# Kernel optimization log

Hardware: AMD Instinct MI355X
Metric: run time of the kernel (lower is better)

The kernel has to match this reference:

```python
import jax, jax.numpy as jnp
import numpy as np
import math

D_MODEL = 1024
NUM_HEAD = 16
HEAD_DIM = D_MODEL // NUM_HEAD
B, S = 4, 2048


def setup_inputs() -> dict:
    key = jax.random.key(0)
    k1, k2, k3, k4, k5 = jax.random.split(key, 5)
    x = jax.random.normal(k1, (B, S, D_MODEL), dtype=jnp.float32)
    # causal mask: True = position masked out
    mask = jnp.triu(jnp.ones((S, S), dtype=bool), k=1)[None, None, :, :]
    sc = 1.0 / math.sqrt(D_MODEL)
    w_q = jax.random.normal(k2, (D_MODEL, D_MODEL), dtype=jnp.float32) * sc
    w_k = jax.random.normal(k3, (D_MODEL, D_MODEL), dtype=jnp.float32) * sc
    w_v = jax.random.normal(k4, (D_MODEL, D_MODEL), dtype=jnp.float32) * sc
    w_out = jax.random.normal(k5, (D_MODEL, D_MODEL), dtype=jnp.float32) * sc
    return {"x": x, "mask": mask, "w_q": w_q, "w_k": w_k, "w_v": w_v, "w_out": w_out}


def reference(x, mask, w_q, w_k, w_v, w_out):
    b, s, _ = x.shape
    # nn.Linear applies x @ W.T; weights stored as [out, in]
    q = jnp.einsum('bsd,ed->bse', x, w_q).reshape(b, s, NUM_HEAD, HEAD_DIM).transpose(0, 2, 1, 3)
    k = jnp.einsum('bsd,ed->bse', x, w_k).reshape(b, s, NUM_HEAD, HEAD_DIM).transpose(0, 2, 1, 3)
    v = jnp.einsum('bsd,ed->bse', x, w_v).reshape(b, s, NUM_HEAD, HEAD_DIM).transpose(0, 2, 1, 3)
    # NOTE: faithful to source - scales by 1/sqrt(d_model), not 1/sqrt(head_dim)
    q = q / jnp.sqrt(jnp.asarray(D_MODEL, dtype=q.dtype))
    attn_weight = jnp.einsum('bhqd,bhkd->bhqk', q, k)  # [B,H,S,S]
    attn_weight = jnp.where(mask, jnp.asarray(-1e9, dtype=attn_weight.dtype), attn_weight)
    attn_weight = jax.nn.softmax(attn_weight, axis=-1)
    attn = jnp.einsum('bhqk,bhkd->bhqd', attn_weight, v)
    attn = attn.transpose(0, 2, 1, 3).reshape(b, s, D_MODEL)
    out = jnp.einsum('bsd,ed->bse', attn, w_out)
    return out
```

## Files before the change

### kernel.cpp

```cpp
#include <hip/hip_runtime.h>

#define BDIM 4
#define SDIM 2048
#define DMODEL 1024
#define NHEAD 16
#define HDIM 64
#define MTOT (BDIM*SDIM)

typedef unsigned short u16;
typedef unsigned int u32;
typedef __attribute__((ext_vector_type(8))) short bf16x8;
typedef __attribute__((ext_vector_type(4))) float f32x4;
typedef __attribute__((ext_vector_type(16))) float f32x16;
typedef __attribute__((ext_vector_type(4))) u32 u32x4;

__device__ __forceinline__ u16 f2bf(float f) {
  unsigned u = __builtin_bit_cast(unsigned, f);
  u += 0x7fffu + ((u >> 16) & 1u);
  return (u16)(u >> 16);
}

__device__ __forceinline__ u32 cvtpk(float a, float b) {
  u32 r;
  asm("v_cvt_pk_bf16_f32 %0, %1, %2" : "=v"(r) : "v"(a), "v"(b));
  return r;
}

__device__ __forceinline__ void gload_lds16(const u16* g, u16* l) {
  __builtin_amdgcn_global_load_lds(
      (const __attribute__((address_space(1))) unsigned int*)g,
      (__attribute__((address_space(3))) unsigned int*)l, 16, 0, 0);
}

__global__ __launch_bounds__(256) void cast_bf16_kernel(
    const float* __restrict__ src, u16* __restrict__ dst, int n4)
{
  const int i = blockIdx.x * 256 + threadIdx.x;
  if (i < n4) {
    const float4 v = reinterpret_cast<const float4*>(src)[i];
    unsigned long long w =
        (unsigned long long)f2bf(v.x)
      | ((unsigned long long)f2bf(v.y) << 16)
      | ((unsigned long long)f2bf(v.z) << 32)
      | ((unsigned long long)f2bf(v.w) << 48);
    reinterpret_cast<unsigned long long*>(dst)[i] = w;
  }
}

__global__ __launch_bounds__(256) void gemm_bf16_kernel(
    const u16* __restrict__ A, const u16* __restrict__ W,
    void* __restrict__ C, float scale, int mode)
{
  __shared__ u16 As[2][128 * 32];
  __shared__ u16 Bs[2][128 * 32];

  const int tid = threadIdx.x;
  const int m0 = blockIdx.y * 128, n0 = blockIdx.x * 128;
  const int l  = tid & 63, wid = tid >> 6;
  const int wr = wid >> 1, wc = wid & 1;
  const int lc = l & 15, lr = l >> 4;
  const int ar = l >> 2;
  const int ac = (l & 3) * 8;

  const f32x4 z4 = {0.f, 0.f, 0.f, 0.f};
  f32x4 acc[4][4];
  #pragma unroll
  for (int i = 0; i < 4; ++i)
    #pragma unroll
    for (int j = 0; j < 4; ++j) acc[i][j] = z4;

  #define GSTAGE(bufi, kk)                                                        \
    { _Pragma("unroll")                                                           \
      for (int j = 0; j < 2; ++j) {                                               \
        const int row = wid * 32 + j * 16;                                        \
        gload_lds16(&A[(size_t)(m0 + row + ar) * DMODEL + (kk) + ac],             \
                    &As[bufi][row * 32]);                                         \
        gload_lds16(&W[(size_t)(n0 + row + ar) * DMODEL + (kk) + ac],             \
                    &Bs[bufi][row * 32]);                                         \
      } }

  GSTAGE(0, 0);
  __syncthreads();

  for (int ks = 0; ks < DMODEL / 32; ++ks) {
    const int cur = ks & 1;
    if (ks + 1 < DMODEL / 32) GSTAGE(cur ^ 1, (ks + 1) * 32);

    bf16x8 a[4], b[4];
    #pragma unroll
    for (int i = 0; i < 4; ++i)
      a[i] = *reinterpret_cast<const bf16x8*>(&As[cur][(wr*64 + i*16 + lc) * 32 + lr*8]);
    #pragma unroll
    for (int j = 0; j < 4; ++j)
      b[j] = *reinterpret_cast<const bf16x8*>(&Bs[cur][(wc*64 + j*16 + lc) * 32 + lr*8]);

    #pragma unroll
    for (int i = 0; i < 4; ++i)
      #pragma unroll
      for (int j = 0; j < 4; ++j)
        acc[i][j] = __builtin_amdgcn_mfma_f32_16x16x32_bf16(a[i], b[j], acc[i][j], 0, 0, 0);
    __syncthreads();
  }
  #undef GSTAGE

  #pragma unroll
  for (int mi = 0; mi < 4; ++mi)
    #pragma unroll
    for (int ni = 0; ni < 4; ++ni) {
      const int col = n0 + wc*64 + ni*16 + lc;
      #pragma unroll
      for (int j = 0; j < 4; ++j) {
        const int row = m0 + wr*64 + mi*16 + lr*4 + j;
        const float v = acc[mi][ni][j] * scale;
        if (mode == 0) {
          reinterpret_cast<float*>(C)[(size_t)row * DMODEL + col] = v;
        } else if (mode == 1) {
          const int b = row >> 11, s = row & (SDIM-1), h = col >> 6, dh = col & 63;
          reinterpret_cast<u16*>(C)[(((size_t)(b*NHEAD + h) * SDIM + s) << 6) + dh] = f2bf(v);
        } else {
          const int b = row >> 11, s = row & (SDIM-1), h = col >> 6, dh = col & 63;
          reinterpret_cast<u16*>(C)[(((size_t)(b*NHEAD + h) * HDIM + dh) << 11) + s] = f2bf(v);
        }
      }
    }
}

__global__ __launch_bounds__(256, 3) void attn_mfma_kernel(
    const u16* __restrict__ Qh, const u16* __restrict__ Kh,
    const u16* __restrict__ Vt, u16* __restrict__ Ob)
{
  __shared__ u16 Ks[2][64 * 64];
  __shared__ u16 Vs[2][64 * 64];

  const int tid = threadIdx.x, l = tid & 63, wid = tid >> 6;
  const int q31 = l & 31, hi = l >> 5;
  const int qt = (int)gridDim.x - 1 - (int)blockIdx.x;
  const int bh = blockIdx.y;
  const size_t base = (size_t)bh * SDIM * HDIM;
  const int qrow0 = qt * 128 + wid * 32;

  const int sr = l >> 3;
  const int sc = ((l & 7) ^ sr) * 8;

  bf16x8 aq[4];
  #pragma unroll
  for (int kc = 0; kc < 4; ++kc)
    aq[kc] = *reinterpret_cast<const bf16x8*>(
        &Qh[base + (size_t)(qrow0 + q31) * HDIM + kc*16 + hi*8]);

  f32x16 o[2], p[2];
  #pragma unroll
  for (int r = 0; r < 16; ++r) { o[0][r] = 0.f; o[1][r] = 0.f; }
  float m_run = -1e30f, l_run = 0.f;

  #define STAGE(bufi, kv0s)                                                     \
    { _Pragma("unroll")                                                         \
      for (int j = 0; j < 2; ++j) {                                             \
        const int rg = wid * 16 + j * 8;                                        \
        gload_lds16(&Kh[base + (size_t)((kv0s) + rg + sr) * HDIM + sc],         \
                    &Ks[bufi][rg * 64]);                                        \
        gload_lds16(&Vt[base + (size_t)(rg + sr) * SDIM + (kv0s) + sc],         \
                    &Vs[bufi][rg * 64]);                                        \
      } }

  const int nt = 2 * qt + 2;
  STAGE(0, 0);
  __syncthreads();

  for (int t = 0; t < nt; ++t) {
    const int kv0 = t * 64;
    const int cur = t & 1;
    if (t + 1 < nt) STAGE(cur ^ 1, kv0 + 64);

    if (kv0 <= qrow0 + 31) {
      #pragma unroll
      for (int kvb = 0; kvb < 2; ++kvb) {
        #pragma unroll
        for (int r = 0; r < 16; ++r) p[kvb][r] = 0.f;
        const int krow = kvb*32 + q31;
        #pragma unroll
        for (int kc = 0; kc < 4; ++kc) {
          const int byte = (krow*128 + kc*32 + hi*16) ^ ((krow & 7) << 4);
          const bf16x8 ak = *reinterpret_cast<const bf16x8*>(
              reinterpret_cast<const char*>(Ks[cur]) + byte);
          p[kvb] = __builtin_amdgcn_mfma_f32_32x32x16_bf16(ak, aq[kc], p[kvb], 0, 0, 0);
        }
      }

      if (kv0 + 63 > qrow0) {
        const int q = qrow0 + q31;
        #pragma unroll
        for (int kvb = 0; kvb < 2; ++kvb)
          #pragma unroll
          for (int r = 0; r < 16; ++r) {
            const int kv = kv0 + kvb*32 + (r & 3) + 8*(r >> 2) + 4*hi;
            if (kv > q) p[kvb][r] = -1e9f;
          }
      }

      float pm = -1e30f;
      #pragma unroll
      for (int r = 0; r < 16; ++r) {
        pm = fmaxf(pm, p[0][r]); pm = fmaxf(pm, p[1][r]);
      }
      pm = fmaxf(pm, __shfl_xor(pm, 32));
      float mn = m_run;
      if (!__all(pm - m_run <= 8.0f)) {
        mn = fmaxf(m_run, pm);
        const float al = __builtin_amdgcn_exp2f(m_run - mn);
        #pragma unroll
        for (int r = 0; r < 16; ++r) { o[0][r] *= al; o[1][r] *= al; }
        l_run *= al;
        m_run = mn;
      }
      float rs = 0.f;
      #pragma unroll
      for (int kvb = 0; kvb < 2; ++kvb)
        #pragma unroll
        for (int r = 0; r < 16; ++r) {
          const float e = __builtin_amdgcn_exp2f(p[kvb][r] - mn);
          p[kvb][r] = e; rs += e;
        }
      rs += __shfl_xor(rs, 32);
      l_run += rs;

      bf16x8 pb[4];
      #pragma unroll
      for (int kvb = 0; kvb < 2; ++kvb)
        #pragma unroll
        for (int s2 = 0; s2 < 2; ++s2) {
          const int rb = s2 * 8;
          const u32 k01 = cvtpk(p[kvb][rb+0], p[kvb][rb+1]);
          const u32 k23 = cvtpk(p[kvb][rb+2], p[kvb][rb+3]);
          const u32 k45 = cvtpk(p[kvb][rb+4], p[kvb][rb+5]);
          const u32 k67 = cvtpk(p[kvb][rb+6], p[kvb][rb+7]);
          const u32 sa = hi ? k01 : k45;
          const u32 sb = hi ? k23 : k67;
          const u32 ra = (u32)__shfl_xor((int)sa, 32);
          const u32 rb2 = (u32)__shfl_xor((int)sb, 32);
          u32x4 w;
          w.x = hi ? ra  : k01;
          w.y = hi ? rb2 : k23;
          w.z = hi ? k45 : ra;
          w.w = hi ? k67 : rb2;
          pb[kvb*2 + s2] = __builtin_bit_cast(bf16x8, w);
        }

      #pragma unroll
      for (int db = 0; db < 2; ++db) {
        const int vrow = db*32 + q31;
        #pragma unroll
        for (int s = 0; s < 4; ++s) {
          const int byte = (vrow*128 + s*32 + hi*16) ^ ((vrow & 7) << 4);
          const bf16x8 av = *reinterpret_cast<const bf16x8*>(
              reinterpret_cast<const char*>(Vs[cur]) + byte);
          o[db] = __builtin_amdgcn_mfma_f32_32x32x16_bf16(av, pb[s], o[db], 0, 0, 0);
        }
      }
    }
    __syncthreads();
  }
  #undef STAGE

  const float inv = 1.0f / l_run;
  char* const myOb = reinterpret_cast<char*>(reinterpret_cast<u16*>(Ks) + wid * 2048);
  #pragma unroll
  for (int db = 0; db < 2; ++db)
    #pragma unroll
    for (int tq = 0; tq < 4; ++tq) {
      const int d0 = db*32 + tq*8 + hi*4;
      uint2 wv;
      wv.x = cvtpk(o[db][tq*4+0] * inv, o[db][tq*4+1] * inv);
      wv.y = cvtpk(o[db][tq*4+2] * inv, o[db][tq*4+3] * inv);
      const int byte = (q31*128 + d0*2) ^ ((q31 & 7) << 4);
      *reinterpret_cast<uint2*>(myOb + byte) = wv;
    }
  __syncthreads();
  const int b = bh >> 4, h = bh & 15;
  const int qr = l >> 1, half = l & 1;
  const int qg = qrow0 + qr;
  #pragma unroll
  for (int i = 0; i < 4; ++i) {
    const int byte = (qr*128 + half*64 + i*16) ^ ((qr & 7) << 4);
    const u32x4 v = *reinterpret_cast<const u32x4*>(myOb + byte);
    *reinterpret_cast<u32x4*>(
        &Ob[((size_t)(b * SDIM + qg)) * DMODEL + h * HDIM + half*32 + i*8]) = v;
  }
}

extern "C" void kernel_launch(void* const* d_in, const int* in_sizes, int n_in,
                              void* d_out, int out_size, void* d_ws, size_t ws_size,
                              hipStream_t stream) {
  const float* x     = (const float*)d_in[0];
  const float* w_q   = (const float*)d_in[2];
  const float* w_k   = (const float*)d_in[3];
  const float* w_v   = (const float*)d_in[4];
  const float* w_out = (const float*)d_in[5];
  float* out = (float*)d_out;

  const size_t NX = (size_t)MTOT * DMODEL;
  const size_t NW = (size_t)DMODEL * DMODEL;
  u16* xb   = (u16*)d_ws;
  u16* wqb  = xb  + NX;
  u16* wkb  = wqb + NW;
  u16* wvb  = wkb + NW;
  u16* wob  = wvb + NW;
  u16* Qhd  = wob + NW;
  u16* Khd  = Qhd + NX;
  u16* Vtd  = Khd + NX;
  u16* attb = Vtd + NX;

  cast_bf16_kernel<<<(int)(NX/4 + 255)/256, 256, 0, stream>>>(x, xb, (int)(NX/4));
  cast_bf16_kernel<<<(int)(NW/4 + 255)/256, 256, 0, stream>>>(w_q,   wqb, (int)(NW/4));
  cast_bf16_kernel<<<(int)(NW/4 + 255)/256, 256, 0, stream>>>(w_k,   wkb, (int)(NW/4));
  cast_bf16_kernel<<<(int)(NW/4 + 255)/256, 256, 0, stream>>>(w_v,   wvb, (int)(NW/4));
  cast_bf16_kernel<<<(int)(NW/4 + 255)/256, 256, 0, stream>>>(w_out, wob, (int)(NW/4));

  const dim3 gg(DMODEL / 128, MTOT / 128);
  gemm_bf16_kernel<<<gg, 256, 0, stream>>>(xb, wqb, Qhd, 1.4426950408889634f / 32.0f, 1);
  gemm_bf16_kernel<<<gg, 256, 0, stream>>>(xb, wkb, Khd, 1.0f, 1);
  gemm_bf16_kernel<<<gg, 256, 0, stream>>>(xb, wvb, Vtd, 1.0f, 2);

  attn_mfma_kernel<<<dim3(SDIM / 128, BDIM * NHEAD), 256, 0, stream>>>(Qhd, Khd, Vtd, attb);

  gemm_bf16_kernel<<<gg, 256, 0, stream>>>(attb, wob, out, 1.0f, 0);
}
```

Measured before the change: 364.1 us.

## Batch weight casts and QKV GEMMs, swizzle tiles, add MFMA priority hints

```diff
diff --git a/kernel.cpp b/kernel.cpp
--- a/kernel.cpp
+++ b/kernel.cpp
@@ -47,15 +47,34 @@
   }
 }
 
-__global__ __launch_bounds__(256) void gemm_bf16_kernel(
+__global__ __launch_bounds__(256) void cast_w4_kernel(
+    const float* __restrict__ w0, const float* __restrict__ w1,
+    const float* __restrict__ w2, const float* __restrict__ w3,
+    u16* __restrict__ d0, u16* __restrict__ d1,
+    u16* __restrict__ d2, u16* __restrict__ d3, int n4)
+{
+  const int y = blockIdx.y;
+  const float* src = (y == 0) ? w0 : (y == 1) ? w1 : (y == 2) ? w2 : w3;
+  u16* dst = (y == 0) ? d0 : (y == 1) ? d1 : (y == 2) ? d2 : d3;
+  const int i = blockIdx.x * 256 + threadIdx.x;
+  if (i < n4) {
+    const float4 v = reinterpret_cast<const float4*>(src)[i];
+    unsigned long long w =
+        (unsigned long long)f2bf(v.x)
+      | ((unsigned long long)f2bf(v.y) << 16)
+      | ((unsigned long long)f2bf(v.z) << 32)
+      | ((unsigned long long)f2bf(v.w) << 48);
+    reinterpret_cast<unsigned long long*>(dst)[i] = w;
+  }
+}
+
+template <int MODE>
+__device__ __forceinline__ void gemm_tile(
     const u16* __restrict__ A, const u16* __restrict__ W,
-    void* __restrict__ C, float scale, int mode)
-{
-  __shared__ u16 As[2][128 * 32];
-  __shared__ u16 Bs[2][128 * 32];
-
+    void* __restrict__ C, float scale, int m0, int n0,
+    u16* As , u16* Bs )
+{
   const int tid = threadIdx.x;
-  const int m0 = blockIdx.y * 128, n0 = blockIdx.x * 128;
   const int l  = tid & 63, wid = tid >> 6;
   const int wr = wid >> 1, wc = wid & 1;
   const int lc = l & 15, lr = l >> 4;
@@ -74,9 +93,9 @@
       for (int j = 0; j < 2; ++j) {                                               \
         const int row = wid * 32 + j * 16;                                        \
         gload_lds16(&A[(size_t)(m0 + row + ar) * DMODEL + (kk) + ac],             \
-                    &As[bufi][row * 32]);                                         \
+                    &As[(bufi) * 4096 + row * 32]);                               \
         gload_lds16(&W[(size_t)(n0 + row + ar) * DMODEL + (kk) + ac],             \
-                    &Bs[bufi][row * 32]);                                         \
+                    &Bs[(bufi) * 4096 + row * 32]);                               \
       } }
 
   GSTAGE(0, 0);
@@ -89,16 +108,18 @@
     bf16x8 a[4], b[4];
     #pragma unroll
     for (int i = 0; i < 4; ++i)
-      a[i] = *reinterpret_cast<const bf16x8*>(&As[cur][(wr*64 + i*16 + lc) * 32 + lr*8]);
+      a[i] = *reinterpret_cast<const bf16x8*>(&As[cur*4096 + (wr*64 + i*16 + lc) * 32 + lr*8]);
     #pragma unroll
     for (int j = 0; j < 4; ++j)
-      b[j] = *reinterpret_cast<const bf16x8*>(&Bs[cur][(wc*64 + j*16 + lc) * 32 + lr*8]);
-
+      b[j] = *reinterpret_cast<const bf16x8*>(&Bs[cur*4096 + (wc*64 + j*16 + lc) * 32 + lr*8]);
+
+    __builtin_amdgcn_s_setprio(1);
     #pragma unroll
     for (int i = 0; i < 4; ++i)
       #pragma unroll
       for (int j = 0; j < 4; ++j)
         acc[i][j] = __builtin_amdgcn_mfma_f32_16x16x32_bf16(a[i], b[j], acc[i][j], 0, 0, 0);
+    __builtin_amdgcn_s_setprio(0);
     __syncthreads();
   }
   #undef GSTAGE
@@ -112,9 +133,9 @@
       for (int j = 0; j < 4; ++j) {
         const int row = m0 + wr*64 + mi*16 + lr*4 + j;
         const float v = acc[mi][ni][j] * scale;
-        if (mode == 0) {
+        if (MODE == 0) {
           reinterpret_cast<float*>(C)[(size_t)row * DMODEL + col] = v;
-        } else if (mode == 1) {
+        } else if (MODE == 1) {
           const int b = row >> 11, s = row & (SDIM-1), h = col >> 6, dh = col & 63;
           reinterpret_cast<u16*>(C)[(((size_t)(b*NHEAD + h) * SDIM + s) << 6) + dh] = f2bf(v);
         } else {
@@ -125,7 +146,40 @@
     }
 }
 
-__global__ __launch_bounds__(256, 3) void attn_mfma_kernel(
+__device__ __forceinline__ void swz_tile(int& m0, int& n0) {
+  const int lin = blockIdx.y * 8 + blockIdx.x;
+  const int swz = (lin & 7) * 64 + (lin >> 3);
+  m0 = (swz >> 3) * 128;
+  n0 = (swz & 7) * 128;
+}
+
+__global__ __launch_bounds__(256) void gemm_qkv_kernel(
+    const u16* __restrict__ xb,
+    const u16* __restrict__ wq, const u16* __restrict__ wk, const u16* __restrict__ wv,
+    u16* __restrict__ Qhd, u16* __restrict__ Khd, u16* __restrict__ Vtd)
+{
+  __shared__ u16 As[2 * 128 * 32];
+  __shared__ u16 Bs[2 * 128 * 32];
+  int m0, n0; swz_tile(m0, n0);
+  const int z = blockIdx.z;
+  if (z == 0)
+    gemm_tile<1>(xb, wq, Qhd, 1.4426950408889634f / 32.0f, m0, n0, As, Bs);
+  else if (z == 1)
+    gemm_tile<1>(xb, wk, Khd, 1.0f, m0, n0, As, Bs);
+  else
+    gemm_tile<2>(xb, wv, Vtd, 1.0f, m0, n0, As, Bs);
+}
+
+__global__ __launch_bounds__(256) void gemm_out_kernel(
+    const u16* __restrict__ A, const u16* __restrict__ W, float* __restrict__ C)
+{
+  __shared__ u16 As[2 * 128 * 32];
+  __shared__ u16 Bs[2 * 128 * 32];
+  int m0, n0; swz_tile(m0, n0);
+  gemm_tile<0>(A, W, C, 1.0f, m0, n0, As, Bs);
+}
+
+__global__ __launch_bounds__(256) void attn_mfma_kernel(
     const u16* __restrict__ Qh, const u16* __restrict__ Kh,
     const u16* __restrict__ Vt, u16* __restrict__ Ob)
 {
@@ -173,6 +227,7 @@
     if (t + 1 < nt) STAGE(cur ^ 1, kv0 + 64);
 
     if (kv0 <= qrow0 + 31) {
+      __builtin_amdgcn_s_setprio(1);
       #pragma unroll
       for (int kvb = 0; kvb < 2; ++kvb) {
         #pragma unroll
@@ -186,6 +241,7 @@
           p[kvb] = __builtin_amdgcn_mfma_f32_32x32x16_bf16(ak, aq[kc], p[kvb], 0, 0, 0);
         }
       }
+      __builtin_amdgcn_s_setprio(0);
 
       if (kv0 + 63 > qrow0) {
         const int q = qrow0 + q31;
@@ -246,6 +302,7 @@
           pb[kvb*2 + s2] = __builtin_bit_cast(bf16x8, w);
         }
 
+      __builtin_amdgcn_s_setprio(1);
       #pragma unroll
       for (int db = 0; db < 2; ++db) {
         const int vrow = db*32 + q31;
@@ -257,6 +314,7 @@
           o[db] = __builtin_amdgcn_mfma_f32_32x32x16_bf16(av, pb[s], o[db], 0, 0, 0);
         }
       }
+      __builtin_amdgcn_s_setprio(0);
     }
     __syncthreads();
   }
@@ -311,17 +369,12 @@
   u16* attb = Vtd + NX;
 
   cast_bf16_kernel<<<(int)(NX/4 + 255)/256, 256, 0, stream>>>(x, xb, (int)(NX/4));
-  cast_bf16_kernel<<<(int)(NW/4 + 255)/256, 256, 0, stream>>>(w_q,   wqb, (int)(NW/4));
-  cast_bf16_kernel<<<(int)(NW/4 + 255)/256, 256, 0, stream>>>(w_k,   wkb, (int)(NW/4));
-  cast_bf16_kernel<<<(int)(NW/4 + 255)/256, 256, 0, stream>>>(w_v,   wvb, (int)(NW/4));
-  cast_bf16_kernel<<<(int)(NW/4 + 255)/256, 256, 0, stream>>>(w_out, wob, (int)(NW/4));
-
-  const dim3 gg(DMODEL / 128, MTOT / 128);
-  gemm_bf16_kernel<<<gg, 256, 0, stream>>>(xb, wqb, Qhd, 1.4426950408889634f / 32.0f, 1);
-  gemm_bf16_kernel<<<gg, 256, 0, stream>>>(xb, wkb, Khd, 1.0f, 1);
-  gemm_bf16_kernel<<<gg, 256, 0, stream>>>(xb, wvb, Vtd, 1.0f, 2);
+  cast_w4_kernel<<<dim3((int)(NW/4 + 255)/256, 4), 256, 0, stream>>>(
+      w_q, w_k, w_v, w_out, wqb, wkb, wvb, wob, (int)(NW/4));
+
+  gemm_qkv_kernel<<<dim3(8, 64, 3), 256, 0, stream>>>(xb, wqb, wkb, wvb, Qhd, Khd, Vtd);
 
   attn_mfma_kernel<<<dim3(SDIM / 128, BDIM * NHEAD), 256, 0, stream>>>(Qhd, Khd, Vtd, attb);
 
-  gemm_bf16_kernel<<<gg, 256, 0, stream>>>(attb, wob, out, 1.0f, 0);
-}
+  gemm_out_kernel<<<dim3(8, 64), 256, 0, stream>>>(attb, wob, out);
+}
```

Result: faster. 325.6 us (-10.6%).
